# Kernel tuning notes

Hardware: AMD Instinct MI355X
Metric: run time of the kernel (lower is better)

Reference implementation:

```python
import jax, jax.numpy as jnp
import numpy as np

B, T, D_IN, D_OUT = 16, 2048, 2048, 2048
N_ADAPTERS, RANK = 8, 16


def setup_inputs() -> dict:
    key = jax.random.key(0)
    k_x, k_w, k_a, k_b, k_s, k_idx = jax.random.split(key, 6)
    x = jax.random.normal(k_x, (B, T, D_IN), dtype=jnp.float32)
    # frozen base weight (nn.Linear stores W as (d_out, d_in)); bias=False
    W = jax.random.normal(k_w, (D_OUT, D_IN), dtype=jnp.float32) * (1.0 / np.sqrt(D_IN))
    # stacked adapter bank: A[a] is (r, d_in), Bm[a] is (d_out, r)
    A = jax.random.normal(k_a, (N_ADAPTERS, RANK, D_IN), dtype=jnp.float32) * 0.02
    Bm = jax.random.normal(k_b, (N_ADAPTERS, D_OUT, RANK), dtype=jnp.float32) * 0.02
    scalings = jnp.ones((N_ADAPTERS,), dtype=jnp.float32)  # alpha / r, pre-merged
    adapter_idx = jax.random.randint(k_idx, (B,), 0, N_ADAPTERS, dtype=jnp.int32)
    return {"x": x, "W": W, "A": A, "Bm": Bm, "scalings": scalings,
            "adapter_idx": adapter_idx}


def reference(x, W, A, Bm, scalings, adapter_idx):
    # base path: H = x @ W^T   -> (B, T, d_out)
    H = jnp.einsum("btd,od->bto", x, W)
    # per-request adapter gather (replaces the Python loop over adapter groups)
    A_b = A[adapter_idx]          # (B, r, d_in)
    B_b = Bm[adapter_idx]         # (B, d_out, r)
    s_b = scalings[adapter_idx]   # (B,)
    # low-rank delta: (x @ A^T) @ B^T, done per request, fully batched
    xa = jnp.einsum("btd,brd->btr", x, A_b)        # (B, T, r)
    delta = jnp.einsum("btr,bor->bto", xa, B_b)    # (B, T, d_out)
    # original computes delta under torch.no_grad() with detached A/B
    delta = jax.lax.stop_gradient(delta * s_b[:, None, None])
    return H + delta
```

## Files before the change

### kernel.cpp

```cpp
#include <hip/hip_runtime.h>
#include <stdint.h>

typedef unsigned short u16;
typedef __attribute__((ext_vector_type(4))) short s16x4;
typedef __attribute__((ext_vector_type(8))) short short8;
typedef __attribute__((ext_vector_type(4))) float f32x4;

static __device__ __forceinline__ u16 f2bf(float f) {
    union { float f; uint32_t u; } c; c.f = f;
    uint32_t u = c.u;
    u += 0x7FFFu + ((u >> 16) & 1u);
    return (u16)(u >> 16);
}

#define D_IN   2048
#define D_OUT  2048
#define MTOT   32768
#define BK     64
#define NTM    32

__device__ __forceinline__ void gload16(const u16* g, u16* l) {
    __builtin_amdgcn_global_load_lds(
        (const __attribute__((address_space(1))) void*)g,
        (__attribute__((address_space(3))) void*)l, 16, 0, 0);
}

__global__ __launch_bounds__(256) void k_prep(
    const float* __restrict__ W, const float* __restrict__ A, const float* __restrict__ Bm,
    u16* __restrict__ Wb, u16* __restrict__ Ap, u16* __restrict__ Bp)
{
    const int b = blockIdx.x, tid = threadIdx.x;
    if (b < 2048) {
        int i = (b * 256 + tid) * 8;
        const float4* p = (const float4*)(W + i);
        float4 v0 = p[0], v1 = p[1];
        short8 o;
        o[0]=f2bf(v0.x); o[1]=f2bf(v0.y); o[2]=f2bf(v0.z); o[3]=f2bf(v0.w);
        o[4]=f2bf(v1.x); o[5]=f2bf(v1.y); o[6]=f2bf(v1.z); o[7]=f2bf(v1.w);
        *(short8*)(Wb + i) = o;
    } else if (b < 6144) {
        int i = (b - 2048) * 256 + tid;
        int d = i & 2047, r = (i >> 11) & 63, a = i >> 17;
        Ap[i] = (r < 16) ? f2bf(A[(((a << 4) + r) << 11) + d]) : (u16)0;
    } else {
        int i = (b - 6144) * 256 + tid;
        int j = i & 63, n = (i >> 6) & 2047, a = i >> 17;
        Bp[i] = (j < 16) ? f2bf(Bm[((((a << 11) + n)) << 4) + j]) : (u16)0;
    }
}

__global__ __launch_bounds__(256) void k_cast_x_xa(
    const float* __restrict__ x, const u16* __restrict__ Ap,
    const float* __restrict__ scal, const int* __restrict__ aidx,
    u16* __restrict__ xb, u16* __restrict__ xa)
{
    __shared__ __align__(16) u16 Xs[128 * BK];
    __shared__ __align__(16) u16 Ps[64 * BK];
    const int tid = threadIdx.x, lane = tid & 63, wid = tid >> 6;
    const int m0 = blockIdx.x << 7;
    const int a = aidx[m0 >> 11];
    const float s = scal[a];
    const int wr = wid >> 1, wc = wid & 1;
    const int arow = (wr << 6) + (lane & 15);
    const int brow = (wc << 5) + (lane & 15);
    const int scol = ((lane & 7) ^ (lane >> 3)) << 3;

    f32x4 acc[4][2];
    #pragma unroll
    for (int i = 0; i < 4; ++i) { acc[i][0] = 0.f; acc[i][1] = 0.f; }

    const int xrow_l = tid >> 4;
    const int xcol   = (tid & 15) << 2;
    const int wslot  = (tid & 15) >> 1;
    const int wsub   = (tid & 1) << 2;

    const u16* apg = Ap + ((size_t)a << 17);
    const u16* gP[2]; u16* lP[2];
    #pragma unroll
    for (int it = 0; it < 2; ++it) {
        const int chunk = (wid << 1) + it;
        const int row = (chunk << 3) + (lane >> 3);
        gP[it] = apg + ((size_t)row << 11) + scol;
        lP[it] = Ps + (chunk << 9) + (lane << 3);
    }

    for (int kt = 0; kt < NTM; ++kt) {
        const int k0 = kt << 6;
        float4 xv[8];
        #pragma unroll
        for (int r = 0; r < 8; ++r)
            xv[r] = *(const float4*)(x + ((size_t)(m0 + (r << 4) + xrow_l) << 11) + k0 + xcol);
        #pragma unroll
        for (int r = 0; r < 8; ++r) {
            const int row = (r << 4) + xrow_l;
            s16x4 c4;
            c4[0]=f2bf(xv[r].x); c4[1]=f2bf(xv[r].y); c4[2]=f2bf(xv[r].z); c4[3]=f2bf(xv[r].w);
            *(s16x4*)(Xs + (row << 6) + ((wslot ^ (row & 7)) << 3) + wsub) = c4;
            *(s16x4*)(xb + ((size_t)(m0 + row) << 11) + k0 + xcol) = c4;
        }
        gload16(gP[0] + k0, lP[0]);
        gload16(gP[1] + k0, lP[1]);
        asm volatile("s_waitcnt vmcnt(0)" ::: "memory");
        __syncthreads();
        #pragma unroll
        for (int kk = 0; kk < 2; ++kk) {
            const int sl = ((kk << 2) + (lane >> 4)) ^ (lane & 7);
            short8 af[4], bv[2];
            #pragma unroll
            for (int mi = 0; mi < 4; ++mi)
                af[mi] = *(const short8*)(Xs + ((arow + mi * 16) << 6) + (sl << 3));
            #pragma unroll
            for (int ni = 0; ni < 2; ++ni)
                bv[ni] = *(const short8*)(Ps + ((brow + ni * 16) << 6) + (sl << 3));
            #pragma unroll
            for (int mi = 0; mi < 4; ++mi)
                #pragma unroll
                for (int ni = 0; ni < 2; ++ni)
                    acc[mi][ni] = __builtin_amdgcn_mfma_f32_16x16x32_bf16(af[mi], bv[ni], acc[mi][ni], 0, 0, 0);
        }
        __syncthreads();
    }

    #pragma unroll
    for (int mi = 0; mi < 4; ++mi) {
        #pragma unroll
        for (int ni = 0; ni < 2; ++ni) {
            const int cc = (wc << 5) + ni * 16 + (lane & 15);
            #pragma unroll
            for (int rr = 0; rr < 4; ++rr) {
                const int mm = m0 + (wr << 6) + mi * 16 + ((lane >> 4) << 2) + rr;
                xa[((size_t)mm << 6) + cc] = f2bf(acc[mi][ni][rr] * s);
            }
        }
    }
}

__global__ __launch_bounds__(512, 2) void k_gemm(
    const u16* __restrict__ xb, const u16* __restrict__ Wb,
    const u16* __restrict__ xa, const u16* __restrict__ Bp,
    const int* __restrict__ aidx, float* __restrict__ out)
{
    __shared__ __align__(16) u16 LDS[2 * 32768];
    const int tid = threadIdx.x, lane = tid & 63, wid = tid >> 6;

    const int newbid = (blockIdx.x & 7) * 128 + (blockIdx.x >> 3);
    const int bm = newbid >> 3, bn = newbid & 7;
    const int m0 = bm << 8, n0 = bn << 8;
    const int wr = wid >> 2, wc = wid & 3;
    const int a = aidx[m0 >> 11];

    f32x4 acc[8][4];
    #pragma unroll
    for (int i = 0; i < 8; ++i)
        #pragma unroll
        for (int j = 0; j < 4; ++j) acc[i][j] = 0.0f;

    const int sc = ((tid & 7) ^ ((tid >> 3) & 7)) << 3;
    const int srw = tid >> 3;

    const int sl0 = (((lane >> 4)    ) ^ (lane & 7)) << 3;
    const int sl1 = (((lane >> 4) + 4) ^ (lane & 7)) << 3;
    const int aRowBase = (wr << 7) + (lane & 15);
    const int bRowBase = (wc << 6) + (lane & 15);

    short8 af[4][2], bv[4][2];

    auto STG = [&](const u16* ptr, int stride, int rowbase, int kofs, int ldsofs) {
        const u16* s_ = ptr + ((size_t)(rowbase + srw)) * stride + kofs + sc;
        gload16(s_,                          &LDS[ldsofs + (tid << 3)]);
        gload16(s_ + ((size_t)stride << 6),  &LDS[ldsofs + 4096 + (tid << 3)]);
    };
    auto SA = [&](int tt, int h) {
        const int lo = ((tt & 1) << 15) + (h << 13);
        if (tt < NTM) STG(xb, 2048, m0 + (h << 7), tt << 6, lo);
        else          STG(xa, 64,   m0 + (h << 7), 0,       lo);
    };
    auto SB = [&](int tt, int h) {
        const int lo = ((tt & 1) << 15) + 16384 + (h << 13);
        if (tt < NTM) STG(Wb, 2048, n0 + (h << 7), tt << 6, lo);
        else          STG(Bp, 64,   (a << 11) + n0 + (h << 7), 0, lo);
    };

    #define BAR  __builtin_amdgcn_s_barrier()
    #define LGK0 do { asm volatile("s_waitcnt lgkmcnt(0)" ::: "memory"); \
                      __builtin_amdgcn_sched_barrier(0); } while (0)

    #define RDA(c_, mq_) do { _Pragma("unroll")                                     \
        for (int mi = 0; mi < 4; ++mi) {                                            \
            const int row = aRowBase + ((mq_) << 6) + (mi << 4);                    \
            af[mi][0] = *(const short8*)&LDS[((c_) << 15) + (row << 6) + sl0];      \
            af[mi][1] = *(const short8*)&LDS[((c_) << 15) + (row << 6) + sl1];      \
        } } while (0)

    #define RDB(c_, ni_) do {                                                       \
            const int row = bRowBase + ((ni_) << 4);                                \
            bv[ni_][0] = *(const short8*)&LDS[((c_) << 15) + 16384 + (row << 6) + sl0]; \
            bv[ni_][1] = *(const short8*)&LDS[((c_) << 15) + 16384 + (row << 6) + sl1]; \
        } while (0)

    #define MM(mq_, ns_) do { __builtin_amdgcn_s_setprio(1); _Pragma("unroll")      \
        for (int kk = 0; kk < 2; ++kk) _Pragma("unroll")                            \
        for (int mi = 0; mi < 4; ++mi) _Pragma("unroll")                            \
        for (int j = 0; j < 2; ++j)                                                 \
            acc[(mq_) * 4 + mi][(ns_) * 2 + j] =                                    \
                __builtin_amdgcn_mfma_f32_16x16x32_bf16(af[mi][kk],                 \
                    bv[(ns_) * 2 + j][kk], acc[(mq_) * 4 + mi][(ns_) * 2 + j], 0, 0, 0); \
        __builtin_amdgcn_s_setprio(0); } while (0)

    SA(0, 0); SA(0, 1); SB(0, 0); SB(0, 1); SB(1, 0); SB(1, 1);
    asm volatile("s_waitcnt vmcnt(4)" ::: "memory");
    BAR;

    for (int t = 0; t <= NTM; ++t) {
        const int c = t & 1;
        RDB(c, 0); RDB(c, 1); RDA(c, 0);
        if (t + 1 <= NTM) SA(t + 1, 0);
        BAR; LGK0; MM(0, 0); BAR;
        RDB(c, 2); RDB(c, 3);
        if (t + 1 <= NTM) SA(t + 1, 1);
        BAR; LGK0; MM(0, 1); BAR;
        RDA(c, 1);
        if (t + 2 <= NTM) SB(t + 2, 0);
        BAR; LGK0; MM(1, 0); BAR;
        if (t + 2 <= NTM) SB(t + 2, 1);
        BAR; MM(1, 1);
        if (t < NTM - 1)      asm volatile("s_waitcnt vmcnt(4)" ::: "memory");
        else if (t == NTM - 1) asm volatile("s_waitcnt vmcnt(0)" ::: "memory");
        BAR;
    }

    #undef MM
    #undef RDB
    #undef RDA
    #undef LGK0
    #undef BAR

    #pragma unroll
    for (int mi = 0; mi < 8; ++mi) {
        #pragma unroll
        for (int ni = 0; ni < 4; ++ni) {
            const int nn = n0 + (wc << 6) + ni * 16 + (lane & 15);
            #pragma unroll
            for (int r = 0; r < 4; ++r) {
                const int mm = m0 + (wr << 7) + mi * 16 + ((lane >> 4) << 2) + r;
                out[((size_t)mm << 11) + nn] = acc[mi][ni][r];
            }
        }
    }
}

extern "C" void kernel_launch(void* const* d_in, const int* in_sizes, int n_in,
                              void* d_out, int out_size, void* d_ws, size_t ws_size,
                              hipStream_t stream) {
    const float* x  = (const float*)d_in[0];
    const float* W  = (const float*)d_in[1];
    const float* A  = (const float*)d_in[2];
    const float* Bm = (const float*)d_in[3];
    const float* sc = (const float*)d_in[4];
    const int* aidx = (const int*)d_in[5];
    float* out = (float*)d_out;

    char* ws = (char*)d_ws;
    u16* xb = (u16*)(ws);
    u16* Wb = (u16*)(ws + 134217728);
    u16* Ap = (u16*)(ws + 134217728 + 8388608);
    u16* Bp = (u16*)(ws + 134217728 + 8388608 + 2097152);
    u16* xa = (u16*)(ws + 134217728 + 8388608 + 2097152 + 2097152);

    hipLaunchKernelGGL(k_prep,      dim3(10240), dim3(256), 0, stream, W, A, Bm, Wb, Ap, Bp);
    hipLaunchKernelGGL(k_cast_x_xa, dim3(256),   dim3(256), 0, stream, x, Ap, sc, aidx, xb, xa);
    hipLaunchKernelGGL(k_gemm,      dim3(1024),  dim3(512), 0, stream, xb, Wb, xa, Bp, aidx, out);
}
```

Measured before the change: 381.9 us.

## Switch GEMM main loop to 32x32x16 MFMA with precomputed load pointers

Replaces the 16x16x32 bf16 MFMA tiling with 32x32x16 MFMAs, so each wave holds 4x2 accumulator blocks of 16 floats and reads A/B fragments as four k-slices per row. This cuts the number of LDS fragment reads and MFMA issues per tile. Global-to-LDS staging addresses are now computed once per base pointer instead of on every stage call, and the LDS swizzle and epilogue row mapping are adapted to the 32x32 output layout. A fragment register layout or swizzle mismatch could cause bank conflicts or wrong results.

Result: slower. 430.8 us (+12.8%).

```diff
diff --git a/kernel.cpp b/kernel.cpp
--- a/kernel.cpp
+++ b/kernel.cpp
@@ -5,6 +5,7 @@
 typedef __attribute__((ext_vector_type(4))) short s16x4;
 typedef __attribute__((ext_vector_type(8))) short short8;
 typedef __attribute__((ext_vector_type(4))) float f32x4;
+typedef __attribute__((ext_vector_type(16))) float f32x16;
 
 static __device__ __forceinline__ u16 f2bf(float f) {
     union { float f; uint32_t u; } c; c.f = f;
@@ -149,101 +150,111 @@
     const int wr = wid >> 2, wc = wid & 3;
     const int a = aidx[m0 >> 11];
 
-    f32x4 acc[8][4];
-    #pragma unroll
-    for (int i = 0; i < 8; ++i)
-        #pragma unroll
-        for (int j = 0; j < 4; ++j) acc[i][j] = 0.0f;
-
-    const int sc = ((tid & 7) ^ ((tid >> 3) & 7)) << 3;
+    f32x16 acc[4][2];
+    #pragma unroll
+    for (int i = 0; i < 4; ++i)
+        #pragma unroll
+        for (int j = 0; j < 2; ++j)
+            #pragma unroll
+            for (int r = 0; r < 16; ++r) acc[i][j][r] = 0.0f;
+
+    const int sc  = ((tid & 7) ^ ((tid >> 3) & 7)) << 3;
     const int srw = tid >> 3;
-
-    const int sl0 = (((lane >> 4)    ) ^ (lane & 7)) << 3;
-    const int sl1 = (((lane >> 4) + 4) ^ (lane & 7)) << 3;
-    const int aRowBase = (wr << 7) + (lane & 15);
-    const int bRowBase = (wc << 6) + (lane & 15);
-
-    short8 af[4][2], bv[4][2];
-
-    auto STG = [&](const u16* ptr, int stride, int rowbase, int kofs, int ldsofs) {
-        const u16* s_ = ptr + ((size_t)(rowbase + srw)) * stride + kofs + sc;
-        gload16(s_,                          &LDS[ldsofs + (tid << 3)]);
-        gload16(s_ + ((size_t)stride << 6),  &LDS[ldsofs + 4096 + (tid << 3)]);
-    };
-    auto SA = [&](int tt, int h) {
-        const int lo = ((tt & 1) << 15) + (h << 13);
-        if (tt < NTM) STG(xb, 2048, m0 + (h << 7), tt << 6, lo);
-        else          STG(xa, 64,   m0 + (h << 7), 0,       lo);
-    };
-    auto SB = [&](int tt, int h) {
-        const int lo = ((tt & 1) << 15) + 16384 + (h << 13);
-        if (tt < NTM) STG(Wb, 2048, n0 + (h << 7), tt << 6, lo);
-        else          STG(Bp, 64,   (a << 11) + n0 + (h << 7), 0, lo);
-    };
+    const u16 *pA[2], *pB[2], *tA[2], *tB[2];
+    #pragma unroll
+    for (int h = 0; h < 2; ++h) {
+        pA[h] = xb + ((size_t)(m0 + (h << 7) + srw) << 11) + sc;
+        pB[h] = Wb + ((size_t)(n0 + (h << 7) + srw) << 11) + sc;
+        tA[h] = xa + ((size_t)(m0 + (h << 7) + srw) << 6) + sc;
+        tB[h] = Bp + ((((size_t)a << 11) + n0 + (h << 7) + srw) << 6) + sc;
+    }
+    const int dbase = tid << 3;
+
+    #define SAm(tt, h, c1) do { const u16* g_ = pA[h] + ((tt) << 6);               \
+        u16* d_ = &LDS[((c1) << 15) + ((h) << 13) + dbase];                         \
+        gload16(g_, d_); gload16(g_ + (64 << 11), d_ + 4096); } while (0)
+    #define SAt(h, c1) do { const u16* g_ = tA[h];                                  \
+        u16* d_ = &LDS[((c1) << 15) + ((h) << 13) + dbase];                         \
+        gload16(g_, d_); gload16(g_ + (64 << 6), d_ + 4096); } while (0)
+    #define SBm(tt, h, c1) do { const u16* g_ = pB[h] + ((tt) << 6);               \
+        u16* d_ = &LDS[((c1) << 15) + 16384 + ((h) << 13) + dbase];                 \
+        gload16(g_, d_); gload16(g_ + (64 << 11), d_ + 4096); } while (0)
+    #define SBt(h, c1) do { const u16* g_ = tB[h];                                  \
+        u16* d_ = &LDS[((c1) << 15) + 16384 + ((h) << 13) + dbase];                 \
+        gload16(g_, d_); gload16(g_ + (64 << 6), d_ + 4096); } while (0)
+
+    const int l31 = lane & 31, h5 = lane >> 5, lw7 = lane & 7;
+    int sl[4];
+    #pragma unroll
+    for (int ks = 0; ks < 4; ++ks) sl[ks] = ((((ks << 1) | h5) ^ lw7) << 3);
+    const int abase = ((wr << 7) + l31) << 6;
+    const int bbase = 16384 + (((wc << 6) + l31) << 6);
+
+    short8 af[2][4], bv[2][4];
+
+    #define RDA2(c_, mlo) do { _Pragma("unroll")                                    \
+        for (int mi = 0; mi < 2; ++mi) _Pragma("unroll")                            \
+        for (int ks = 0; ks < 4; ++ks)                                              \
+            af[mi][ks] = *(const short8*)&LDS[((c_) << 15) + abase +                \
+                                              (((mlo) + mi) << 11) + sl[ks]]; } while (0)
+    #define RDB1(c_, nb) do { _Pragma("unroll")                                     \
+        for (int ks = 0; ks < 4; ++ks)                                              \
+            bv[nb][ks] = *(const short8*)&LDS[((c_) << 15) + bbase +                \
+                                              ((nb) << 11) + sl[ks]]; } while (0)
 
     #define BAR  __builtin_amdgcn_s_barrier()
-    #define LGK0 do { asm volatile("s_waitcnt lgkmcnt(0)" ::: "memory"); \
+    #define LGK0 do { asm volatile("s_waitcnt lgkmcnt(0)" ::: "memory");            \
                       __builtin_amdgcn_sched_barrier(0); } while (0)
 
-    #define RDA(c_, mq_) do { _Pragma("unroll")                                     \
-        for (int mi = 0; mi < 4; ++mi) {                                            \
-            const int row = aRowBase + ((mq_) << 6) + (mi << 4);                    \
-            af[mi][0] = *(const short8*)&LDS[((c_) << 15) + (row << 6) + sl0];      \
-            af[mi][1] = *(const short8*)&LDS[((c_) << 15) + (row << 6) + sl1];      \
-        } } while (0)
-
-    #define RDB(c_, ni_) do {                                                       \
-            const int row = bRowBase + ((ni_) << 4);                                \
-            bv[ni_][0] = *(const short8*)&LDS[((c_) << 15) + 16384 + (row << 6) + sl0]; \
-            bv[ni_][1] = *(const short8*)&LDS[((c_) << 15) + 16384 + (row << 6) + sl1]; \
-        } while (0)
-
-    #define MM(mq_, ns_) do { __builtin_amdgcn_s_setprio(1); _Pragma("unroll")      \
-        for (int kk = 0; kk < 2; ++kk) _Pragma("unroll")                            \
-        for (int mi = 0; mi < 4; ++mi) _Pragma("unroll")                            \
-        for (int j = 0; j < 2; ++j)                                                 \
-            acc[(mq_) * 4 + mi][(ns_) * 2 + j] =                                    \
-                __builtin_amdgcn_mfma_f32_16x16x32_bf16(af[mi][kk],                 \
-                    bv[(ns_) * 2 + j][kk], acc[(mq_) * 4 + mi][(ns_) * 2 + j], 0, 0, 0); \
+    #define MM2(mlo, nb) do { __builtin_amdgcn_s_setprio(1); _Pragma("unroll")      \
+        for (int ks = 0; ks < 4; ++ks) _Pragma("unroll")                            \
+        for (int mi = 0; mi < 2; ++mi)                                              \
+            acc[(mlo) + mi][nb] = __builtin_amdgcn_mfma_f32_32x32x16_bf16(          \
+                af[mi][ks], bv[nb][ks], acc[(mlo) + mi][nb], 0, 0, 0);              \
         __builtin_amdgcn_s_setprio(0); } while (0)
 
-    SA(0, 0); SA(0, 1); SB(0, 0); SB(0, 1); SB(1, 0); SB(1, 1);
+    SAm(0, 0, 0); SAm(0, 1, 0); SBm(0, 0, 0); SBm(0, 1, 0); SBm(1, 0, 1); SBm(1, 1, 1);
     asm volatile("s_waitcnt vmcnt(4)" ::: "memory");
     BAR;
 
     for (int t = 0; t <= NTM; ++t) {
         const int c = t & 1;
-        RDB(c, 0); RDB(c, 1); RDA(c, 0);
-        if (t + 1 <= NTM) SA(t + 1, 0);
-        BAR; LGK0; MM(0, 0); BAR;
-        RDB(c, 2); RDB(c, 3);
-        if (t + 1 <= NTM) SA(t + 1, 1);
-        BAR; LGK0; MM(0, 1); BAR;
-        RDA(c, 1);
-        if (t + 2 <= NTM) SB(t + 2, 0);
-        BAR; LGK0; MM(1, 0); BAR;
-        if (t + 2 <= NTM) SB(t + 2, 1);
-        BAR; MM(1, 1);
-        if (t < NTM - 1)      asm volatile("s_waitcnt vmcnt(4)" ::: "memory");
+        RDB1(c, 0); RDA2(c, 0);
+        if (t + 1 < NTM) SAm(t + 1, 0, c ^ 1); else if (t + 1 == NTM) SAt(0, c ^ 1);
+        BAR; LGK0; MM2(0, 0); BAR;
+        RDB1(c, 1);
+        if (t + 1 < NTM) SAm(t + 1, 1, c ^ 1); else if (t + 1 == NTM) SAt(1, c ^ 1);
+        BAR; LGK0; MM2(0, 1); BAR;
+        RDA2(c, 2);
+        if (t + 2 < NTM) SBm(t + 2, 0, c); else if (t + 2 == NTM) SBt(0, c);
+        BAR; LGK0; MM2(2, 0); BAR;
+        if (t + 2 < NTM) SBm(t + 2, 1, c); else if (t + 2 == NTM) SBt(1, c);
+        BAR; MM2(2, 1);
+        if (t < NTM - 1)       asm volatile("s_waitcnt vmcnt(4)" ::: "memory");
         else if (t == NTM - 1) asm volatile("s_waitcnt vmcnt(0)" ::: "memory");
         BAR;
     }
 
-    #undef MM
-    #undef RDB
-    #undef RDA
+    #undef MM2
     #undef LGK0
     #undef BAR
-
-    #pragma unroll
-    for (int mi = 0; mi < 8; ++mi) {
-        #pragma unroll
-        for (int ni = 0; ni < 4; ++ni) {
-            const int nn = n0 + (wc << 6) + ni * 16 + (lane & 15);
-            #pragma unroll
-            for (int r = 0; r < 4; ++r) {
-                const int mm = m0 + (wr << 7) + mi * 16 + ((lane >> 4) << 2) + r;
-                out[((size_t)mm << 11) + nn] = acc[mi][ni][r];
+    #undef RDB1
+    #undef RDA2
+    #undef SBt
+    #undef SBm
+    #undef SAt
+    #undef SAm
+
+    #pragma unroll
+    for (int mb = 0; mb < 4; ++mb) {
+        #pragma unroll
+        for (int nb = 0; nb < 2; ++nb) {
+            const int nn = n0 + (wc << 6) + (nb << 5) + l31;
+            #pragma unroll
+            for (int r = 0; r < 16; ++r) {
+                const int row = (r & 3) + ((r >> 2) << 3) + (h5 << 2);
+                const int mm = m0 + (wr << 7) + (mb << 5) + row;
+                out[((size_t)mm << 11) + nn] = acc[mb][nb][r];
             }
         }
     }
```
